# Optimization experiments

Measured on AMD Instinct MI355X. Metric: run time of the kernel, lower is better.

The kernel has to match this reference:

```python
import jax, jax.numpy as jnp
import numpy as np

EMB = 1024
HEADS = 8
SEQ = 4096
LN_EPS = 1e-5


def _layernorm(x, g, b):
    mu = jnp.mean(x, axis=-1, keepdims=True)
    var = jnp.mean(jnp.square(x - mu), axis=-1, keepdims=True)
    return (x - mu) * jax.lax.rsqrt(var + LN_EPS) * g + b


def setup_inputs() -> dict:
    key = jax.random.key(0)
    ks = jax.random.split(key, 12)
    s = 1.0 / np.sqrt(EMB)
    sz = 1.0 / np.sqrt(EMB * HEADS)
    return {
        "history": jax.random.normal(ks[0], (SEQ, EMB), jnp.float32),
        "embdding": jax.random.normal(ks[1], (SEQ, EMB), jnp.float32),
        # per-head Linear weights, torch layout [out, in], stacked over heads
        "Wq_w": jax.random.uniform(ks[2], (HEADS, EMB, EMB), jnp.float32, -s, s),
        "Wq_b": jax.random.uniform(ks[3], (HEADS, EMB), jnp.float32, -s, s),
        "Wk_w": jax.random.uniform(ks[4], (HEADS, EMB, EMB), jnp.float32, -s, s),
        "Wk_b": jax.random.uniform(ks[5], (HEADS, EMB), jnp.float32, -s, s),
        "Wv_w": jax.random.uniform(ks[6], (HEADS, EMB, EMB), jnp.float32, -s, s),
        "Wv_b": jax.random.uniform(ks[7], (HEADS, EMB), jnp.float32, -s, s),
        "Wz_w": jax.random.uniform(ks[8], (EMB, EMB * HEADS), jnp.float32, -sz, sz),
        "Wz_b": jax.random.uniform(ks[9], (EMB,), jnp.float32, -sz, sz),
        "ln1_g": jnp.ones((EMB,), jnp.float32),
        "ln1_b": jnp.zeros((EMB,), jnp.float32),
        "Wf_w": jax.random.uniform(ks[10], (EMB, EMB), jnp.float32, -s, s),
        "Wf_b": jax.random.uniform(ks[11], (EMB,), jnp.float32, -s, s),
        "ln2_g": jnp.ones((EMB,), jnp.float32),
        "ln2_b": jnp.zeros((EMB,), jnp.float32),
    }


def reference(history, embdding, Wq_w, Wq_b, Wk_w, Wk_b, Wv_w, Wv_b,
              Wz_w, Wz_b, ln1_g, ln1_b, Wf_w, Wf_b, ln2_g, ln2_b):
    S, E = embdding.shape
    H = Wq_w.shape[0]
    # per-head linears (torch: y = x @ W.T + b), batched over heads
    Q = jnp.einsum('se,hfe->hsf', embdding, Wq_w) + Wq_b[:, None, :]  # [H,S,E]
    K = jnp.einsum('se,hfe->hsf', embdding, Wk_w) + Wk_b[:, None, :]
    V = jnp.einsum('se,hfe->hsf', history, Wv_w) + Wv_b[:, None, :]
    # K^T @ Q -> [H, E, E], softmax over dim=1 of the 2D matrix == last axis here
    scores = jnp.einsum('hse,hsf->hef', K, Q) / jnp.sqrt(jnp.asarray(E, Q.dtype))
    A = jax.nn.softmax(scores, axis=-1)  # [H,E,E]
    Zh = jnp.einsum('hse,hef->hsf', V, A)  # [H,S,E]
    Z = jnp.transpose(Zh, (1, 0, 2)).reshape(S, H * E)  # cat(dim=1) in head order
    O = Z @ Wz_w.T + Wz_b  # [S,E]
    LN1 = _layernorm(O, ln1_g, ln1_b) + embdding
    FN = LN1 @ Wf_w.T + Wf_b
    LN2 = _layernorm(FN, ln2_g, ln2_b) + LN1
    return LN2
```

## Files before the change

### kernel.cpp

```cpp
#include <hip/hip_runtime.h>


constexpr int EMB = 1024;
constexpr int SEQ = 4096;
constexpr int NH  = 8;

using f32x4  = __attribute__((ext_vector_type(4))) float;
using bf16x8 = __attribute__((ext_vector_type(8))) __bf16;
using us8    = __attribute__((ext_vector_type(8))) unsigned short;
using us4    = __attribute__((ext_vector_type(4))) unsigned short;

#define GLOAD_LDS16(g, l) __builtin_amdgcn_global_load_lds(                 \
    (const __attribute__((address_space(1))) void*)(g),                     \
    (__attribute__((address_space(3))) void*)(l), 16, 0, 0)

__device__ inline unsigned short f2bf(float x) {
  unsigned int u = __float_as_uint(x);
  u += 0x7FFFu + ((u >> 16) & 1u);
  return (unsigned short)(u >> 16);
}
__device__ inline float bf2f(unsigned short h) {
  return __uint_as_float(((unsigned int)h) << 16);
}
__device__ inline f32x4 ntl4(const float* p) {
  return __builtin_nontemporal_load((const f32x4*)p);
}
__device__ inline us4 cvt4(f32x4 x) {
  us4 o; o[0] = f2bf(x[0]); o[1] = f2bf(x[1]); o[2] = f2bf(x[2]); o[3] = f2bf(x[3]);
  return o;
}

template <int MODE>
__device__ __attribute__((always_inline)) void gemm_body(
    unsigned short* lds, int wg,
    const unsigned short* A, const unsigned short* B, void* Cout,
    int K, int lda, int ldb, int ldc,
    long long aZ, long long bZ, long long cZ, int nx, int ny,
    const float* e0, const float* e1, const float* e2, const float* e3) {
  const int bx = wg % nx;
  const int by = (wg / nx) % ny;
  const int z  = wg / (nx * ny);
  A += (size_t)z * aZ;
  B += (size_t)z * bZ;
  const int tid = threadIdx.x;
  const int lane = tid & 63, wid = tid >> 6;
  const int wm = wid >> 1, wn = wid & 1;
  const int row0 = bx * 64, col0 = by * 128;

  unsigned short* As = lds;
  unsigned short* Bs = lds + 64 * 64;

  f32x4 acc[2][4] = {};
  const int lrow = lane & 15, kg = lane >> 4;
  const int lr = lane >> 3;
  const int lc = (lane & 7) * 8;

  const int nt = K >> 6;
  for (int t = 0; t < nt; ++t) {
    const int k0 = t << 6;
#pragma unroll
    for (int c = 0; c < 2; ++c) {
      int chunk = wid * 2 + c;
      int r = chunk * 8 + lr;
      GLOAD_LDS16(A + (size_t)(row0 + r) * lda + k0 + lc, &As[chunk * 512]);
    }
#pragma unroll
    for (int c = 0; c < 4; ++c) {
      int chunk = wid * 4 + c;
      int r = chunk * 8 + lr;
      GLOAD_LDS16(B + (size_t)(col0 + r) * ldb + k0 + lc, &Bs[chunk * 512]);
    }
    __syncthreads();
#pragma unroll
    for (int ks = 0; ks < 2; ++ks) {
      bf16x8 a[2], b[4];
      int koff = ks * 32 + kg * 8;
#pragma unroll
      for (int i = 0; i < 2; ++i)
        a[i] = *(const bf16x8*)&As[(wm * 32 + i * 16 + lrow) * 64 + koff];
#pragma unroll
      for (int j = 0; j < 4; ++j)
        b[j] = *(const bf16x8*)&Bs[(wn * 64 + j * 16 + lrow) * 64 + koff];
#pragma unroll
      for (int i = 0; i < 2; ++i)
#pragma unroll
        for (int j = 0; j < 4; ++j)
          acc[i][j] = __builtin_amdgcn_mfma_f32_16x16x32_bf16(a[i], b[j], acc[i][j], 0, 0, 0);
    }
    __syncthreads();
  }

  const int rb = (lane >> 4) * 4, cc = lane & 15;
  if (MODE == 1 || MODE == 4) {
    unsigned short* Cs = lds;
#pragma unroll
    for (int i = 0; i < 2; ++i) {
#pragma unroll
      for (int j = 0; j < 4; ++j) {
#pragma unroll
        for (int r = 0; r < 4; ++r) {
          float val = acc[i][j][r];
          int mm = wm * 32 + i * 16 + rb + r;
          int nn = wn * 64 + j * 16 + cc;
          if (MODE == 4) {
            int m = row0 + mm, n = col0 + nn;
            float bq = e0[z * EMB + m], uu = e1[z * EMB + n];
            float bk = e2[z * EMB + n], vv = e3[z * EMB + m];
            val = (val + bq * (uu + (float)SEQ * bk) + vv * bk) * (1.0f / 32.0f);
          }
          Cs[mm * 128 + nn] = f2bf(val);
        }
      }
    }
    __syncthreads();
    unsigned short* Cg = (unsigned short*)Cout + (size_t)z * cZ;
#pragma unroll
    for (int p = 0; p < 4; ++p) {
      int idx = p * 256 + tid;
      int row = idx >> 4, col = (idx & 15) * 8;
      *(us8*)(Cg + (size_t)(row0 + row) * ldc + col0 + col) =
          *(const us8*)&Cs[row * 128 + col];
    }
  } else {
#pragma unroll
    for (int i = 0; i < 2; ++i) {
#pragma unroll
      for (int j = 0; j < 4; ++j) {
#pragma unroll
        for (int r = 0; r < 4; ++r) {
          int m = row0 + wm * 32 + i * 16 + rb + r;
          int n = col0 + wn * 64 + j * 16 + cc;
          size_t off = (size_t)z * cZ + (size_t)m * ldc + n;
          ((float*)Cout)[off] = acc[i][j][r] + e0[n];
        }
      }
    }
  }
}

template <int MODE>
__global__ __launch_bounds__(256) void gemm_nt(const unsigned short* __restrict__ A,
                                               const unsigned short* __restrict__ B,
                                               void* __restrict__ Cout,
                                               int K, int lda, int ldb, int ldc,
                                               long long aZ, long long bZ, long long cZ,
                                               int nx, int ny,
                                               const float* __restrict__ e0,
                                               const float* __restrict__ e1,
                                               const float* __restrict__ e2,
                                               const float* __restrict__ e3) {
  __shared__ __align__(16) unsigned short lds[(64 + 128) * 64];
  const int q = gridDim.x >> 3;
  const int wg = (blockIdx.x & 7) * q + (blockIdx.x >> 3);
  gemm_body<MODE>(lds, wg, A, B, Cout, K, lda, ldb, ldc, aZ, bZ, cZ, nx, ny,
                  e0, e1, e2, e3);
}

__global__ __launch_bounds__(256) void colsum_xt_k(const float* __restrict__ emb,
                                                   const float* __restrict__ Wv,
                                                   float* __restrict__ part,
                                                   unsigned short* __restrict__ XT,
                                                   unsigned short* __restrict__ WvT) {
  __shared__ float tileT[64][65];
  const int b = blockIdx.x, tid = threadIdx.x;
  if (b < 128) {
    int e = (b & 3) * 256 + tid;
    int y = b >> 2;
    float s = 0.f;
    for (int r = y * 128; r < y * 128 + 128; ++r) s += emb[(size_t)r * EMB + e];
    part[y * EMB + e] = s;
    return;
  }
  const float* src; unsigned short* dst; int R, r0, c0;
  if (b < 1152) {
    int tb = b - 128;
    src = emb; dst = XT; R = SEQ;
    r0 = (tb >> 4) * 64; c0 = (tb & 15) * 64;
  } else {
    int t2 = b - 1152, z = t2 >> 8, tt = t2 & 255;
    src = Wv + (size_t)z * EMB * EMB; dst = WvT + (size_t)z * EMB * EMB;
    R = EMB;
    r0 = (tt >> 4) * 64; c0 = (tt & 15) * 64;
  }
  int tx = tid & 15, ty = tid >> 4;
#pragma unroll
  for (int p = 0; p < 4; ++p) {
    int ir = p * 16 + ty;
    f32x4 x = ntl4(src + (size_t)(r0 + ir) * EMB + c0 + tx * 4);
    tileT[tx * 4 + 0][ir] = x[0]; tileT[tx * 4 + 1][ir] = x[1];
    tileT[tx * 4 + 2][ir] = x[2]; tileT[tx * 4 + 3][ir] = x[3];
  }
  __syncthreads();
#pragma unroll
  for (int p = 0; p < 4; ++p) {
    int orow = p * 16 + ty;
    f32x4 x;
    x[0] = tileT[orow][tx * 4 + 0]; x[1] = tileT[orow][tx * 4 + 1];
    x[2] = tileT[orow][tx * 4 + 2]; x[3] = tileT[orow][tx * 4 + 3];
    *(us4*)(dst + (size_t)(c0 + orow) * R + r0 + tx * 4) = cvt4(x);
  }
}

__global__ __launch_bounds__(256) void colsum_red_k(const float* __restrict__ part,
                                                    float* __restrict__ xbar) {
  int e = blockIdx.x * 256 + threadIdx.x;
  float s = 0.f;
  for (int y = 0; y < 32; ++y) s += part[y * EMB + e];
  xbar[e] = s;
}

__global__ __launch_bounds__(256) void gram_cvt_k(
    const unsigned short* __restrict__ XT, unsigned short* __restrict__ Gp,
    const float* __restrict__ Wk, const float* __restrict__ Wq,
    const float* __restrict__ hist, const float* __restrict__ Wz,
    const float* __restrict__ Wf, const float* __restrict__ xbar,
    unsigned short* __restrict__ Wkb, unsigned short* __restrict__ Wqb,
    unsigned short* __restrict__ Yb, unsigned short* __restrict__ Wzb,
    unsigned short* __restrict__ Wfb,
    float* __restrict__ u, float* __restrict__ v) {
  __shared__ __align__(16) unsigned short smem[(64 + 128) * 64];
  const int tid = threadIdx.x;
  if (blockIdx.x < 1024) {
    const int wg = ((int)blockIdx.x & 7) * 128 + ((int)blockIdx.x >> 3);
    gemm_body<1>(smem, wg, XT, XT, Gp, 512, SEQ, SEQ, EMB,
                 512, 512, (long long)EMB * EMB, 16, 8,
                 nullptr, nullptr, nullptr, nullptr);
    return;
  }
  int b2 = blockIdx.x - 1024;
  if (b2 < 4096) {
    int gw = b2 * 4 + (tid >> 6);
    int lane = tid & 63;
    const float* src = (gw < 8192) ? Wk : Wq;
    unsigned short* dst = (gw < 8192) ? Wkb : Wqb;
    float* dot = (gw < 8192) ? u : v;
    int row = gw & 8191;
    const float* sr = src + (size_t)row * EMB;
    const float4* xb4 = (const float4*)xbar;
    unsigned short* dr = dst + (size_t)row * EMB;
    float s = 0.f;
#pragma unroll
    for (int j = 0; j < 4; ++j) {
      int idx = j * 64 + lane;
      f32x4 x = ntl4(sr + idx * 4);
      float4 xb = xb4[idx];
      *(us4*)(dr + idx * 4) = cvt4(x);
      s += x[0] * xb.x + x[1] * xb.y + x[2] * xb.z + x[3] * xb.w;
    }
#pragma unroll
    for (int off = 32; off; off >>= 1) s += __shfl_down(s, off);
    if (lane == 0) dot[row] = s;
  } else {
    size_t f0 = (size_t)(b2 - 4096) * 8192;
    const float* src; unsigned short* dst; size_t loc;
    if (f0 < 4194304ull) { src = hist; dst = Yb; loc = f0; }
    else if (f0 < 12582912ull) { src = Wz; dst = Wzb; loc = f0 - 4194304ull; }
    else { src = Wf; dst = Wfb; loc = f0 - 12582912ull; }
#pragma unroll
    for (int p = 0; p < 8; ++p) {
      int i = p * 256 + tid;
      f32x4 x = ntl4(src + loc + i * 4);
      *(us4*)(dst + loc + i * 4) = cvt4(x);
    }
  }
}

__global__ __launch_bounds__(256) void mp_dvec_k(
    const unsigned short* __restrict__ Cbf, const unsigned short* __restrict__ Wzb,
    unsigned short* __restrict__ Mp,
    const float* __restrict__ bz, const float* __restrict__ cvec,
    float* __restrict__ d) {
  __shared__ __align__(16) unsigned short smem[(64 + 128) * 64];
  const int tid = threadIdx.x;
  if (blockIdx.x < 1024) {
    const int wg = ((int)blockIdx.x & 7) * 128 + ((int)blockIdx.x >> 3);
    gemm_body<1>(smem, wg, Cbf, Wzb, Mp, EMB, EMB, NH * EMB, EMB,
                 (long long)EMB * EMB, (long long)EMB, (long long)EMB * EMB, 16, 8,
                 nullptr, nullptr, nullptr, nullptr);
    return;
  }
  int g = blockIdx.x - 1024;
  float* sb = (float*)smem;
  const unsigned short* row = Wzb + (size_t)g * (NH * EMB);
  float s = 0.f;
#pragma unroll
  for (int p = 0; p < 4; ++p) {
    int i = p * 256 + tid;
    us8 w = ((const us8*)row)[i];
    float4 c0 = ((const float4*)cvec)[i * 2];
    float4 c1 = ((const float4*)cvec)[i * 2 + 1];
    s += bf2f(w[0]) * c0.x + bf2f(w[1]) * c0.y + bf2f(w[2]) * c0.z + bf2f(w[3]) * c0.w;
    s += bf2f(w[4]) * c1.x + bf2f(w[5]) * c1.y + bf2f(w[6]) * c1.z + bf2f(w[7]) * c1.w;
  }
  int lane = tid & 63, w = tid >> 6;
#pragma unroll
  for (int off = 32; off; off >>= 1) s += __shfl_down(s, off);
  if (lane == 0) sb[w] = s;
  __syncthreads();
  if (tid == 0) d[g] = bz[g] + sb[0] + sb[1] + sb[2] + sb[3];
}

__global__ __launch_bounds__(256) void mred_tr_k(const unsigned short* __restrict__ Mp,
                                                 unsigned short* __restrict__ MT) {
  __shared__ float t[32][33];
  int g0 = blockIdx.x * 32, e0 = blockIdx.y * 32;
  int tx = threadIdx.x & 31, ty = threadIdx.x >> 5;
#pragma unroll
  for (int k = 0; k < 4; ++k) {
    int e = e0 + ty + k * 8;
    float s = 0.f;
#pragma unroll
    for (int h = 0; h < NH; ++h)
      s += bf2f(Mp[((size_t)h << 20) + (size_t)e * EMB + g0 + tx]);
    t[ty + k * 8][tx] = s;
  }
  __syncthreads();
#pragma unroll
  for (int k = 0; k < 4; ++k) {
    int r = ty + k * 8;
    MT[(size_t)(g0 + r) * EMB + e0 + tx] = f2bf(t[tx][r]);
  }
}

__global__ __launch_bounds__(256) void gram_red_k(const unsigned short* __restrict__ Gp,
                                                  unsigned short* __restrict__ Gbf) {
  int i = blockIdx.x * 256 + threadIdx.x;
  float4 s = {0.f, 0.f, 0.f, 0.f};
#pragma unroll
  for (int z = 0; z < 8; ++z) {
    ushort4 v = ((const ushort4*)(Gp + (size_t)z * EMB * EMB))[i];
    s.x += bf2f(v.x); s.y += bf2f(v.y); s.z += bf2f(v.z); s.w += bf2f(v.w);
  }
  ushort4 o; o.x = f2bf(s.x); o.y = f2bf(s.y); o.z = f2bf(s.z); o.w = f2bf(s.w);
  ((ushort4*)Gbf)[i] = o;
}

__global__ __launch_bounds__(256) void colstat1_k(const unsigned short* __restrict__ ScT,
                                                  float* __restrict__ m_part,
                                                  float* __restrict__ s_part) {
  int col = blockIdx.x * 256 + threadIdx.x;
  int rc = blockIdx.y, h = blockIdx.z;
  const unsigned short* base = ScT + ((size_t)h * EMB + rc * 64) * EMB + col;
  float m = -1e30f, s = 0.f;
#pragma unroll 4
  for (int r = 0; r < 64; ++r) {
    float x = bf2f(base[(size_t)r * EMB]);
    float nm = fmaxf(m, x);
    s = s * __expf(m - nm) + __expf(x - nm);
    m = nm;
  }
  m_part[((size_t)h * 16 + rc) * EMB + col] = m;
  s_part[((size_t)h * 16 + rc) * EMB + col] = s;
}

__global__ __launch_bounds__(256) void colstat2_k(const float* __restrict__ m_part,
                                                  const float* __restrict__ s_part,
                                                  float* __restrict__ mfin,
                                                  float* __restrict__ isfin) {
  int i = blockIdx.x * 256 + threadIdx.x;
  int h = i >> 10, col = i & 1023;
  float M = -1e30f, S = 0.f;
#pragma unroll
  for (int c = 0; c < 16; ++c) {
    float m = m_part[((size_t)h * 16 + c) * EMB + col];
    float s = s_part[((size_t)h * 16 + c) * EMB + col];
    float nm = fmaxf(M, m);
    S = S * __expf(M - nm) + s * __expf(m - nm);
    M = nm;
  }
  mfin[i] = M;
  isfin[i] = 1.0f / S;
}

__global__ __launch_bounds__(256) void at_cvec_k(const unsigned short* __restrict__ ScT,
                                                 const float* __restrict__ mfin,
                                                 const float* __restrict__ isfin,
                                                 const float* __restrict__ bv,
                                                 unsigned short* __restrict__ AT,
                                                 float* __restrict__ cbuf) {
  __shared__ float sb[4];
  int f = blockIdx.x, h = blockIdx.y, tid = threadIdx.x;
  size_t rowoff = ((size_t)h * EMB + f) * EMB;
  ushort4 xr = ((const ushort4*)(ScT + rowoff))[tid];
  float4 m  = ((const float4*)(mfin + (size_t)h * EMB))[tid];
  float4 is = ((const float4*)(isfin + (size_t)h * EMB))[tid];
  float4 b  = ((const float4*)(bv + (size_t)h * EMB))[tid];
  float a0 = __expf(bf2f(xr.x) - m.x) * is.x;
  float a1 = __expf(bf2f(xr.y) - m.y) * is.y;
  float a2 = __expf(bf2f(xr.z) - m.z) * is.z;
  float a3 = __expf(bf2f(xr.w) - m.w) * is.w;
  ushort4 o; o.x = f2bf(a0); o.y = f2bf(a1); o.z = f2bf(a2); o.w = f2bf(a3);
  ((ushort4*)(AT + rowoff))[tid] = o;
  float s = a0 * b.x + a1 * b.y + a2 * b.z + a3 * b.w;
  int lane = tid & 63, w = tid >> 6;
#pragma unroll
  for (int off = 32; off; off >>= 1) s += __shfl_down(s, off);
  if (lane == 0) sb[w] = s;
  __syncthreads();
  if (tid == 0) cbuf[h * EMB + f] = sb[0] + sb[1] + sb[2] + sb[3];
}

__global__ __launch_bounds__(256) void layernorm_k(const float* __restrict__ Xin,
                                                   const float* __restrict__ resid,
                                                   const float* __restrict__ gw,
                                                   const float* __restrict__ bw,
                                                   float* __restrict__ outf,
                                                   unsigned short* __restrict__ outb) {
  __shared__ float sb[16];
  int row = blockIdx.x, tid = threadIdx.x;
  float4 v = ((const float4*)(Xin + (size_t)row * EMB))[tid];
  float s = v.x + v.y + v.z + v.w;
  float q = v.x * v.x + v.y * v.y + v.z * v.z + v.w * v.w;
  int lane = tid & 63, w = tid >> 6;
#pragma unroll
  for (int off = 32; off; off >>= 1) { s += __shfl_down(s, off); q += __shfl_down(q, off); }
  if (lane == 0) { sb[w] = s; sb[8 + w] = q; }
  __syncthreads();
  float mu  = (sb[0] + sb[1] + sb[2] + sb[3]) * (1.0f / EMB);
  float var = (sb[8] + sb[9] + sb[10] + sb[11]) * (1.0f / EMB) - mu * mu;
  float rs = rsqrtf(var + 1e-5f);
  float4 rv = ((const float4*)(resid + (size_t)row * EMB))[tid];
  float4 gv = ((const float4*)gw)[tid];
  float4 bv = ((const float4*)bw)[tid];
  float o0 = (v.x - mu) * rs * gv.x + bv.x + rv.x;
  float o1 = (v.y - mu) * rs * gv.y + bv.y + rv.y;
  float o2 = (v.z - mu) * rs * gv.z + bv.z + rv.z;
  float o3 = (v.w - mu) * rs * gv.w + bv.w + rv.w;
  float4 ov; ov.x = o0; ov.y = o1; ov.z = o2; ov.w = o3;
  ((float4*)(outf + (size_t)row * EMB))[tid] = ov;
  if (outb) {
    ushort4 ob; ob.x = f2bf(o0); ob.y = f2bf(o1); ob.z = f2bf(o2); ob.w = f2bf(o3);
    ((ushort4*)(outb + (size_t)row * EMB))[tid] = ob;
  }
}

extern "C" void kernel_launch(void* const* d_in, const int* in_sizes, int n_in,
                              void* d_out, int out_size, void* d_ws, size_t ws_size,
                              hipStream_t stream) {
  const float* history = (const float*)d_in[0];
  const float* emb     = (const float*)d_in[1];
  const float* Wq_w = (const float*)d_in[2];
  const float* Wq_b = (const float*)d_in[3];
  const float* Wk_w = (const float*)d_in[4];
  const float* Wk_b = (const float*)d_in[5];
  const float* Wv_w = (const float*)d_in[6];
  const float* Wv_b = (const float*)d_in[7];
  const float* Wz_w = (const float*)d_in[8];
  const float* Wz_b = (const float*)d_in[9];
  const float* ln1_g = (const float*)d_in[10];
  const float* ln1_b = (const float*)d_in[11];
  const float* Wf_w = (const float*)d_in[12];
  const float* Wf_b = (const float*)d_in[13];
  const float* ln2_g = (const float*)d_in[14];
  const float* ln2_b = (const float*)d_in[15];

  char* ws = (char*)d_ws;
  const size_t MB = 1024ull * 1024ull;
  unsigned short* XT  = (unsigned short*)(ws + 0);
  unsigned short* Ybf = (unsigned short*)(ws + 8 * MB);
  unsigned short* Wkb = (unsigned short*)(ws + 16 * MB);
  unsigned short* Wqb = (unsigned short*)(ws + 32 * MB);
  unsigned short* WvT = (unsigned short*)(ws + 48 * MB);
  unsigned short* Wzb = (unsigned short*)(ws + 64 * MB);
  unsigned short* Wfb = (unsigned short*)(ws + 80 * MB);
  unsigned short* Gbf = (unsigned short*)(ws + 82 * MB);
  float* xpart = (float*)(ws + 84 * MB);
  float* xbar  = (float*)(ws + 84 * MB + 160 * 1024);
  float* ubuf  = (float*)(ws + 84 * MB + 192 * 1024);
  float* vbuf  = (float*)(ws + 84 * MB + 256 * 1024);
  float* cbuf  = (float*)(ws + 84 * MB + 320 * 1024);
  float* dbuf  = (float*)(ws + 84 * MB + 384 * 1024);
  unsigned short* Tbf = (unsigned short*)(ws + 85 * MB);
  float* Sc  = (float*)(ws + 101 * MB);
  char*  St  = ws + 133 * MB;
  unsigned short* ATb = (unsigned short*)(ws + 149 * MB);
  unsigned short* MTb = (unsigned short*)(ws + 165 * MB);
  float* m_part = (float*)(St);
  float* s_part = (float*)(St + 512 * 1024);
  float* mfin   = (float*)(St + 1024 * 1024);
  float* isfin  = (float*)(St + 1056 * 1024);
  unsigned short* Gp  = (unsigned short*)Sc;
  unsigned short* ScT = (unsigned short*)Sc;
  unsigned short* Cbf = Tbf;
  unsigned short* Mp  = (unsigned short*)Sc;
  float* Obuf = (float*)St;
  float* LN1  = (float*)ATb;
  unsigned short* LN1b = XT;
  float* FN   = (float*)Tbf;
  const long long EE = (long long)EMB * EMB;

  colsum_xt_k<<<dim3(3200), 256, 0, stream>>>(emb, Wv_w, xpart, XT, WvT);
  colsum_red_k<<<dim3(4), 256, 0, stream>>>(xpart, xbar);

  gram_cvt_k<<<dim3(6784), 256, 0, stream>>>(XT, Gp,
                                             Wk_w, Wq_w, history, Wz_w, Wf_w,
                                             xbar,
                                             Wkb, Wqb, Ybf, Wzb, Wfb,
                                             ubuf, vbuf);
  gram_red_k<<<dim3(EMB * EMB / 4 / 256), 256, 0, stream>>>(Gp, Gbf);
  gemm_nt<1><<<dim3(1024), 256, 0, stream>>>(Wqb, Gbf, Tbf, EMB, EMB, EMB, EMB,
                                             EE, 0, EE, 16, 8,
                                             nullptr, nullptr, nullptr, nullptr);
  gemm_nt<4><<<dim3(1024), 256, 0, stream>>>(Tbf, Wkb, ScT, EMB, EMB, EMB, EMB,
                                             EE, EE, EE, 16, 8,
                                             Wq_b, ubuf, Wk_b, vbuf);
  colstat1_k<<<dim3(4, 16, NH), 256, 0, stream>>>(ScT, m_part, s_part);
  colstat2_k<<<dim3(32), 256, 0, stream>>>(m_part, s_part, mfin, isfin);
  at_cvec_k<<<dim3(EMB, NH), 256, 0, stream>>>(ScT, mfin, isfin, Wv_b, ATb, cbuf);
  gemm_nt<1><<<dim3(1024), 256, 0, stream>>>(WvT, ATb, Cbf, EMB, EMB, EMB, EMB,
                                             EE, EE, EE, 16, 8,
                                             nullptr, nullptr, nullptr, nullptr);
  mp_dvec_k<<<dim3(2048), 256, 0, stream>>>(Cbf, Wzb, Mp, Wz_b, cbuf, dbuf);
  mred_tr_k<<<dim3(EMB / 32, EMB / 32), 256, 0, stream>>>(Mp, MTb);
  gemm_nt<3><<<dim3(512), 256, 0, stream>>>(Ybf, MTb, Obuf, EMB, EMB, EMB, EMB,
                                            0, 0, 0, 64, 8,
                                            dbuf, nullptr, nullptr, nullptr);
  layernorm_k<<<dim3(SEQ), 256, 0, stream>>>(Obuf, emb, ln1_g, ln1_b, LN1, LN1b);
  gemm_nt<3><<<dim3(512), 256, 0, stream>>>(LN1b, Wfb, FN, EMB, EMB, EMB, EMB,
                                            0, 0, 0, 64, 8,
                                            Wf_b, nullptr, nullptr, nullptr);
  layernorm_k<<<dim3(SEQ), 256, 0, stream>>>(FN, LN1, ln2_g, ln2_b, (float*)d_out, nullptr);
}
```

Measured before the change: 281.6 us.

## Double-buffer GEMM LDS tiles to overlap global loads with MFMA compute

The shared GEMM body now uses two LDS buffers. It issues the async global->LDS loads for tile t+1 before computing tile t and waits with an explicit vmcnt on only the older loads, so memory latency overlaps the MFMA work. This doubles the LDS footprint of every kernel that uses gemm_body, which may lower occupancy, and it depends on a hand-tuned vmcnt count matching the six loads issued per stage.

```diff
diff --git a/kernel.cpp b/kernel.cpp
--- a/kernel.cpp
+++ b/kernel.cpp
@@ -47,17 +47,14 @@
   const int wm = wid >> 1, wn = wid & 1;
   const int row0 = bx * 64, col0 = by * 128;
 
-  unsigned short* As = lds;
-  unsigned short* Bs = lds + 64 * 64;
-
   f32x4 acc[2][4] = {};
   const int lrow = lane & 15, kg = lane >> 4;
   const int lr = lane >> 3;
   const int lc = (lane & 7) * 8;
 
-  const int nt = K >> 6;
-  for (int t = 0; t < nt; ++t) {
-    const int k0 = t << 6;
+  auto stage = [&](int buf, int k0) {
+    unsigned short* As = lds + buf * 12288;
+    unsigned short* Bs = As + 4096;
 #pragma unroll
     for (int c = 0; c < 2; ++c) {
       int chunk = wid * 2 + c;
@@ -70,7 +67,22 @@
       int r = chunk * 8 + lr;
       GLOAD_LDS16(B + (size_t)(col0 + r) * ldb + k0 + lc, &Bs[chunk * 512]);
     }
-    __syncthreads();
+  };
+
+  const int nt = K >> 6;
+  stage(0, 0);
+  for (int t = 0; t < nt; ++t) {
+    const int cur = t & 1;
+    if (t + 1 < nt) {
+      stage(cur ^ 1, (t + 1) << 6);
+      asm volatile("s_waitcnt vmcnt(6)" ::: "memory");
+    } else {
+      asm volatile("s_waitcnt vmcnt(0)" ::: "memory");
+    }
+    __builtin_amdgcn_s_barrier();
+    asm volatile("" ::: "memory");
+    const unsigned short* As = lds + cur * 12288;
+    const unsigned short* Bs = As + 4096;
 #pragma unroll
     for (int ks = 0; ks < 2; ++ks) {
       bf16x8 a[2], b[4];
@@ -87,7 +99,9 @@
         for (int j = 0; j < 4; ++j)
           acc[i][j] = __builtin_amdgcn_mfma_f32_16x16x32_bf16(a[i], b[j], acc[i][j], 0, 0, 0);
     }
-    __syncthreads();
+    asm volatile("" ::: "memory");
+    __builtin_amdgcn_s_barrier();
+    asm volatile("" ::: "memory");
   }
 
   const int rb = (lane >> 4) * 4, cc = lane & 15;
@@ -149,7 +163,7 @@
                                                const float* __restrict__ e1,
                                                const float* __restrict__ e2,
                                                const float* __restrict__ e3) {
-  __shared__ __align__(16) unsigned short lds[(64 + 128) * 64];
+  __shared__ __align__(16) unsigned short lds[2 * (64 + 128) * 64];
   const int q = gridDim.x >> 3;
   const int wg = (blockIdx.x & 7) * q + (blockIdx.x >> 3);
   gemm_body<MODE>(lds, wg, A, B, Cout, K, lda, ldb, ldc, aZ, bZ, cZ, nx, ny,
@@ -218,7 +232,7 @@
     unsigned short* __restrict__ Yb, unsigned short* __restrict__ Wzb,
     unsigned short* __restrict__ Wfb,
     float* __restrict__ u, float* __restrict__ v) {
-  __shared__ __align__(16) unsigned short smem[(64 + 128) * 64];
+  __shared__ __align__(16) unsigned short smem[2 * (64 + 128) * 64];
   const int tid = threadIdx.x;
   if (blockIdx.x < 1024) {
     const int wg = ((int)blockIdx.x & 7) * 128 + ((int)blockIdx.x >> 3);
@@ -270,7 +284,7 @@
     unsigned short* __restrict__ Mp,
     const float* __restrict__ bz, const float* __restrict__ cvec,
     float* __restrict__ d) {
-  __shared__ __align__(16) unsigned short smem[(64 + 128) * 64];
+  __shared__ __align__(16) unsigned short smem[2 * (64 + 128) * 64];
   const int tid = threadIdx.x;
   if (blockIdx.x < 1024) {
     const int wg = ((int)blockIdx.x & 7) * 128 + ((int)blockIdx.x >> 3);
```

New measurement: 281.1 us. Within noise of the previous version (-0.2%).

## Fuse column softmax partial stats into scores GEMM epilogue and interleave fused-kernel blocks

Applied to the files above, without the earlier changes.

The scores GEMM (MODE 4) now computes per-tile column max and sum-of-exp from the bf16 tile in LDS and writes the softmax partials directly, which removes the separate colstat1 kernel and its re-read of the score matrix. The gram_cvt and mp_dvec kernels also interleave their GEMM blocks with conversion/dot blocks in the block index order, instead of putting all GEMM blocks first, so compute-bound and memory-bound work are spread across the device together. This adds some epilogue work and exp calls to every GEMM tile.

```diff
diff --git a/kernel.cpp b/kernel.cpp
--- a/kernel.cpp
+++ b/kernel.cpp
@@ -36,7 +36,8 @@
     const unsigned short* A, const unsigned short* B, void* Cout,
     int K, int lda, int ldb, int ldc,
     long long aZ, long long bZ, long long cZ, int nx, int ny,
-    const float* e0, const float* e1, const float* e2, const float* e3) {
+    const float* e0, const float* e1, const float* e2, const float* e3,
+    float* mpart, float* spart) {
   const int bx = wg % nx;
   const int by = (wg / nx) % ny;
   const int z  = wg / (nx * ny);
@@ -121,6 +122,24 @@
       *(us8*)(Cg + (size_t)(row0 + row) * ldc + col0 + col) =
           *(const us8*)&Cs[row * 128 + col];
     }
+    if (MODE == 4) {
+      int colx = tid >> 1, half = tid & 1;
+      float mx = -1e30f;
+#pragma unroll 8
+      for (int r = 0; r < 32; ++r)
+        mx = fmaxf(mx, bf2f(Cs[(half * 32 + r) * 128 + colx]));
+      mx = fmaxf(mx, __shfl_xor(mx, 1));
+      float se = 0.f;
+#pragma unroll 8
+      for (int r = 0; r < 32; ++r)
+        se += __expf(bf2f(Cs[(half * 32 + r) * 128 + colx]) - mx);
+      se += __shfl_xor(se, 1);
+      if (half == 0) {
+        size_t soff = ((size_t)z * 16 + bx) * EMB + col0 + colx;
+        mpart[soff] = mx;
+        spart[soff] = se;
+      }
+    }
   } else {
 #pragma unroll
     for (int i = 0; i < 2; ++i) {
@@ -148,12 +167,14 @@
                                                const float* __restrict__ e0,
                                                const float* __restrict__ e1,
                                                const float* __restrict__ e2,
-                                               const float* __restrict__ e3) {
+                                               const float* __restrict__ e3,
+                                               float* __restrict__ mpart,
+                                               float* __restrict__ spart) {
   __shared__ __align__(16) unsigned short lds[(64 + 128) * 64];
   const int q = gridDim.x >> 3;
   const int wg = (blockIdx.x & 7) * q + (blockIdx.x >> 3);
   gemm_body<MODE>(lds, wg, A, B, Cout, K, lda, ldb, ldc, aZ, bZ, cZ, nx, ny,
-                  e0, e1, e2, e3);
+                  e0, e1, e2, e3, mpart, spart);
 }
 
 __global__ __launch_bounds__(256) void colsum_xt_k(const float* __restrict__ emb,
@@ -220,16 +241,23 @@
     float* __restrict__ u, float* __restrict__ v) {
   __shared__ __align__(16) unsigned short smem[(64 + 128) * 64];
   const int tid = threadIdx.x;
-  if (blockIdx.x < 1024) {
-    const int wg = ((int)blockIdx.x & 7) * 128 + ((int)blockIdx.x >> 3);
-    gemm_body<1>(smem, wg, XT, XT, Gp, 512, SEQ, SEQ, EMB,
-                 512, 512, (long long)EMB * EMB, 16, 8,
-                 nullptr, nullptr, nullptr, nullptr);
-    return;
-  }
-  int b2 = blockIdx.x - 1024;
-  if (b2 < 4096) {
-    int gw = b2 * 4 + (tid >> 6);
+  const int bx = blockIdx.x;
+  int c;
+  if (bx < 6144) {
+    int q6 = bx / 6, r6 = bx - q6 * 6;
+    if (r6 == 0) {
+      const int wg = (q6 & 7) * 128 + (q6 >> 3);
+      gemm_body<1>(smem, wg, XT, XT, Gp, 512, SEQ, SEQ, EMB,
+                   512, 512, (long long)EMB * EMB, 16, 8,
+                   nullptr, nullptr, nullptr, nullptr, nullptr, nullptr);
+      return;
+    }
+    c = q6 * 5 + r6 - 1;
+  } else {
+    c = 5120 + (bx - 6144);
+  }
+  if (c < 4096) {
+    int gw = c * 4 + (tid >> 6);
     int lane = tid & 63;
     const float* src = (gw < 8192) ? Wk : Wq;
     unsigned short* dst = (gw < 8192) ? Wkb : Wqb;
@@ -251,7 +279,7 @@
     for (int off = 32; off; off >>= 1) s += __shfl_down(s, off);
     if (lane == 0) dot[row] = s;
   } else {
-    size_t f0 = (size_t)(b2 - 4096) * 8192;
+    size_t f0 = (size_t)(c - 4096) * 8192;
     const float* src; unsigned short* dst; size_t loc;
     if (f0 < 4194304ull) { src = hist; dst = Yb; loc = f0; }
     else if (f0 < 12582912ull) { src = Wz; dst = Wzb; loc = f0 - 4194304ull; }
@@ -272,14 +300,16 @@
     float* __restrict__ d) {
   __shared__ __align__(16) unsigned short smem[(64 + 128) * 64];
   const int tid = threadIdx.x;
-  if (blockIdx.x < 1024) {
-    const int wg = ((int)blockIdx.x & 7) * 128 + ((int)blockIdx.x >> 3);
+  const int bx = blockIdx.x;
+  if ((bx & 1) == 0) {
+    int g = bx >> 1;
+    const int wg = (g & 7) * 128 + (g >> 3);
     gemm_body<1>(smem, wg, Cbf, Wzb, Mp, EMB, EMB, NH * EMB, EMB,
                  (long long)EMB * EMB, (long long)EMB, (long long)EMB * EMB, 16, 8,
-                 nullptr, nullptr, nullptr, nullptr);
+                 nullptr, nullptr, nullptr, nullptr, nullptr, nullptr);
     return;
   }
-  int g = blockIdx.x - 1024;
+  int g = bx >> 1;
   float* sb = (float*)smem;
   const unsigned short* row = Wzb + (size_t)g * (NH * EMB);
   float s = 0.f;
@@ -333,24 +363,6 @@
   }
   ushort4 o; o.x = f2bf(s.x); o.y = f2bf(s.y); o.z = f2bf(s.z); o.w = f2bf(s.w);
   ((ushort4*)Gbf)[i] = o;
-}
-
-__global__ __launch_bounds__(256) void colstat1_k(const unsigned short* __restrict__ ScT,
-                                                  float* __restrict__ m_part,
-                                                  float* __restrict__ s_part) {
-  int col = blockIdx.x * 256 + threadIdx.x;
-  int rc = blockIdx.y, h = blockIdx.z;
-  const unsigned short* base = ScT + ((size_t)h * EMB + rc * 64) * EMB + col;
-  float m = -1e30f, s = 0.f;
-#pragma unroll 4
-  for (int r = 0; r < 64; ++r) {
-    float x = bf2f(base[(size_t)r * EMB]);
-    float nm = fmaxf(m, x);
-    s = s * __expf(m - nm) + __expf(x - nm);
-    m = nm;
-  }
-  m_part[((size_t)h * 16 + rc) * EMB + col] = m;
-  s_part[((size_t)h * 16 + rc) * EMB + col] = s;
 }
 
 __global__ __launch_bounds__(256) void colstat2_k(const float* __restrict__ m_part,
@@ -500,24 +512,28 @@
   gram_red_k<<<dim3(EMB * EMB / 4 / 256), 256, 0, stream>>>(Gp, Gbf);
   gemm_nt<1><<<dim3(1024), 256, 0, stream>>>(Wqb, Gbf, Tbf, EMB, EMB, EMB, EMB,
                                              EE, 0, EE, 16, 8,
-                                             nullptr, nullptr, nullptr, nullptr);
+                                             nullptr, nullptr, nullptr, nullptr,
+                                             nullptr, nullptr);
   gemm_nt<4><<<dim3(1024), 256, 0, stream>>>(Tbf, Wkb, ScT, EMB, EMB, EMB, EMB,
                                              EE, EE, EE, 16, 8,
-                                             Wq_b, ubuf, Wk_b, vbuf);
-  colstat1_k<<<dim3(4, 16, NH), 256, 0, stream>>>(ScT, m_part, s_part);
+                                             Wq_b, ubuf, Wk_b, vbuf,
+                                             m_part, s_part);
   colstat2_k<<<dim3(32), 256, 0, stream>>>(m_part, s_part, mfin, isfin);
   at_cvec_k<<<dim3(EMB, NH), 256, 0, stream>>>(ScT, mfin, isfin, Wv_b, ATb, cbuf);
   gemm_nt<1><<<dim3(1024), 256, 0, stream>>>(WvT, ATb, Cbf, EMB, EMB, EMB, EMB,
                                              EE, EE, EE, 16, 8,
-                                             nullptr, nullptr, nullptr, nullptr);
+                                             nullptr, nullptr, nullptr, nullptr,
+                                             nullptr, nullptr);
   mp_dvec_k<<<dim3(2048), 256, 0, stream>>>(Cbf, Wzb, Mp, Wz_b, cbuf, dbuf);
   mred_tr_k<<<dim3(EMB / 32, EMB / 32), 256, 0, stream>>>(Mp, MTb);
   gemm_nt<3><<<dim3(512), 256, 0, stream>>>(Ybf, MTb, Obuf, EMB, EMB, EMB, EMB,
                                             0, 0, 0, 64, 8,
-                                            dbuf, nullptr, nullptr, nullptr);
+                                            dbuf, nullptr, nullptr, nullptr,
+                                            nullptr, nullptr);
   layernorm_k<<<dim3(SEQ), 256, 0, stream>>>(Obuf, emb, ln1_g, ln1_b, LN1, LN1b);
   gemm_nt<3><<<dim3(512), 256, 0, stream>>>(LN1b, Wfb, FN, EMB, EMB, EMB, EMB,
                                             0, 0, 0, 64, 8,
-                                            Wf_b, nullptr, nullptr, nullptr);
+                                            Wf_b, nullptr, nullptr, nullptr,
+                                            nullptr, nullptr);
   layernorm_k<<<dim3(SEQ), 256, 0, stream>>>(FN, LN1, ln2_g, ln2_b, (float*)d_out, nullptr);
 }
```

New measurement: 308.9 us. 1.1x slower.
